# Performance work log

Hardware: AMD Instinct MI355X
Metric: run time of the kernel (lower is better)

The kernel has to match this reference:

```python
import jax, jax.numpy as jnp
import numpy as np

N_NODES = 65536
VOCAB = 1000
IN_DIM = 256
MEM_DIM = 256
HIDDEN = 256
NUM_CLASSES = 2


def _rand_parents(rng, n):
    # parent[i] < i for i >= 1 ; node 0 is the root (parent entry unused/masked)
    p = np.zeros(n, dtype=np.int64)
    p[1:] = rng.integers(0, np.arange(1, n))
    return jnp.asarray(p, dtype=jnp.int32)


def setup_inputs() -> dict:
    key = jax.random.key(0)
    ks = jax.random.split(key, 16)
    rng = np.random.default_rng(0)
    s = 0.05
    return {
        "l_tokens": jax.random.randint(ks[0], (N_NODES,), 0, VOCAB, dtype=jnp.int32),
        "l_parent": _rand_parents(rng, N_NODES),
        "r_tokens": jax.random.randint(ks[1], (N_NODES,), 0, VOCAB, dtype=jnp.int32),
        "r_parent": _rand_parents(rng, N_NODES),
        "emb_W": jax.random.normal(ks[2], (VOCAB, IN_DIM), jnp.float32) * s,
        "Wioux": jax.random.normal(ks[3], (IN_DIM, 3 * MEM_DIM), jnp.float32) * s,
        "bioux": jax.random.normal(ks[4], (3 * MEM_DIM,), jnp.float32) * s,
        "Wiouh": jax.random.normal(ks[5], (MEM_DIM, 3 * MEM_DIM), jnp.float32) * s,
        "biouh": jax.random.normal(ks[6], (3 * MEM_DIM,), jnp.float32) * s,
        "Wfx": jax.random.normal(ks[7], (IN_DIM, MEM_DIM), jnp.float32) * s,
        "bfx": jax.random.normal(ks[8], (MEM_DIM,), jnp.float32) * s,
        "Wfh": jax.random.normal(ks[9], (MEM_DIM, MEM_DIM), jnp.float32) * s,
        "bfh": jax.random.normal(ks[10], (MEM_DIM,), jnp.float32) * s,
        "Wh": jax.random.normal(ks[11], (2 * MEM_DIM, HIDDEN), jnp.float32) * s,
        "bh": jax.random.normal(ks[12], (HIDDEN,), jnp.float32) * s,
        "Wp": jax.random.normal(ks[13], (HIDDEN, NUM_CLASSES), jnp.float32) * s,
        "bp": jax.random.normal(ks[14], (NUM_CLASSES,), jnp.float32) * s,
    }


def _tree_lstm_root_c(tokens, parent, emb_W, Wioux, bioux, Wiouh, biouh,
                      Wfx, bfx, Wfh, bfh):
    # Batched x-dependent projections (faithful: ioux(emb), fx(emb))
    X = emb_W[tokens]                       # [N, in_dim]
    ioux_all = X @ Wioux + bioux            # [N, 3M]
    fx_all = X @ Wfx + bfx                  # [N, M]
    n = tokens.shape[0]
    m = Wfh.shape[0]

    def step(carry, i):
        h_sum, fc_sum, c_root = carry
        # ChildSumTreeLSTM.node_forward for node i
        iou = ioux_all[i] + h_sum[i] @ Wiouh + biouh
        ig, og, ug = jnp.split(iou, 3)
        c = jax.nn.sigmoid(ig) * jnp.tanh(ug) + fc_sum[i]   # leaf: fc_sum=0, h_sum=0
        h = jax.nn.sigmoid(og) * jnp.tanh(c)
        # forget-gate contribution of node i to its parent p:
        p = parent[i]
        f = jax.nn.sigmoid(h @ Wfh + bfh + fx_all[p])
        mask = (i != 0).astype(h.dtype)      # root has no parent
        h_sum = h_sum.at[p].add(h * mask)
        fc_sum = fc_sum.at[p].add(f * c * mask)
        c_root = jnp.where(i == 0, c, c_root)
        return (h_sum, fc_sum, c_root), None

    init = (jnp.zeros((n, m), X.dtype), jnp.zeros((n, m), X.dtype),
            jnp.zeros((m,), X.dtype))
    # children-before-parents order: descending index (parent[i] < i)
    (h_sum, fc_sum, c_root), _ = jax.lax.scan(step, init, jnp.arange(n - 1, -1, -1))
    return c_root                            # lstate == root cell state c


def reference(l_tokens, l_parent, r_tokens, r_parent, emb_W, Wioux, bioux,
              Wiouh, biouh, Wfx, bfx, Wfh, bfh, Wh, bh, Wp, bp):
    cl = _tree_lstm_root_c(l_tokens, l_parent, emb_W, Wioux, bioux, Wiouh,
                           biouh, Wfx, bfx, Wfh, bfh)
    cr = _tree_lstm_root_c(r_tokens, r_parent, emb_W, Wioux, bioux, Wiouh,
                           biouh, Wfx, bfx, Wfh, bfh)
    # Similarity head on root cell states
    vec = jnp.concatenate([cl * cr, jnp.abs(cl - cr)])[None, :]  # [1, 2M]
    hid = jax.nn.sigmoid(vec @ Wh + bh)
    return jax.nn.softmax(hid @ Wp + bp, axis=1)                 # [1, num_classes]
```

## Files before the change

### kernel.cpp

```cpp
#include <hip/hip_runtime.h>
#include <math.h>

#define NN 65536
#define TWO_N (2 * NN)
#define VOCAB 1000
#define MD 256
#define G3 768
#define DMAX 65536
#define HALF (DMAX / 2)
#define DCAP 128
#define NB 64
#define NT 256
#define NTS 1024
#define NSPAN 1024
#define SPAN 128
#define NTEAMS 64

typedef __attribute__((ext_vector_type(8))) short bf16x8;
typedef __attribute__((ext_vector_type(4))) float f32x4;

struct Params {
    const int* l_tokens; const int* l_parent;
    const int* r_tokens; const int* r_parent;
    const float* emb_W;
    const float* Wioux; const float* bioux;
    const float* Wiouh; const float* biouh;
    const float* Wfx;   const float* bfx;
    const float* Wfh;   const float* bfh;
    const float* Wh;    const float* bh;
    const float* Wp;    const float* bp;
    float* out;
    float* E_ioux;
    float* E_fx;
    float* C_leaf;
    float* H_leaf;
    float* FH_leaf;
    unsigned int* Wiouh_p;
    unsigned int* Wfh_p;
    float* h_sum;
    float* fc_sum;
    float* c_root;
    unsigned short* hstage;
    int* tarr;
    int* anc_a; int* anc_b; int* dep_a; int* dep_b;
    int* hc;
    int* pending;
    int* pend2;
    int* rank;
    int* blocksum;
    int* cnt; int* offs; int* cur;
    int* order;
    int* lorder;
    int* lstart;
    int* gtab;
    int* gdb;
    int* ecut;
    int* dbase;
    int* maxd;
    int cap_rows;
};

struct SWT {
    unsigned int wiou[12 * 2048];
    unsigned short hbufA[NB * MD];
    int nid[NB]; int row[NB]; int prow[NB]; int tok[NB]; int ptok[NB];
    int pgid[NB];
};

__device__ __forceinline__ float sigmoidf_(float x) {
    return 1.0f / (1.0f + __expf(-x));
}
__device__ __forceinline__ float tanhf_(float x) {
    float ex = __expf(2.0f * x);
    return 1.0f - 2.0f / (ex + 1.0f);
}
__device__ __forceinline__ unsigned int bf16rne_(float x) {
    unsigned int b = __float_as_uint(x);
    return (b + 0x7FFFu + ((b >> 16) & 1u)) >> 16;
}
__device__ __forceinline__ int aload_(int* p) {
    return __hip_atomic_load(p, __ATOMIC_RELAXED, __HIP_MEMORY_SCOPE_AGENT);
}
__device__ __forceinline__ float acohf_(const float* p) {
    return __hip_atomic_load((float*)p, __ATOMIC_RELAXED,
                             __HIP_MEMORY_SCOPE_AGENT);
}
__device__ __forceinline__ unsigned long long acohu64_(const void* p) {
    return __hip_atomic_load((unsigned long long*)p, __ATOMIC_RELAXED,
                             __HIP_MEMORY_SCOPE_AGENT);
}
__device__ __forceinline__ int rowr(const Params& P, int tree, int d, int lr) {
    int r = P.dbase[tree * HALF + d] + lr;
    if (r >= P.cap_rows) r -= P.cap_rows;
    return r;
}

__global__ __launch_bounds__(NT) void k_prep(Params P) {
    __shared__ float es[4][MD];
    const int t = threadIdx.x, bid = blockIdx.x, nblk = gridDim.x;
    const int gsize = nblk * NT, gtid = bid * NT + t;
    for (int u = gtid; u < 48 * 2048; u += gsize) {
        int tl = u >> 11, rem = u & 2047;
        int kb = rem >> 8, rem2 = rem & 255;
        int ln = rem2 >> 2, jj = (rem2 & 3) << 1;
        int k = kb * 32 + (ln >> 4) * 8 + jj;
        int n = tl * 16 + (ln & 15);
        float x0 = P.Wiouh[(size_t)k * G3 + n];
        float x1 = P.Wiouh[(size_t)(k + 1) * G3 + n];
        P.Wiouh_p[u] = bf16rne_(x0) | (bf16rne_(x1) << 16);
    }
    for (int u = gtid; u < 16 * 2048; u += gsize) {
        int tl = u >> 11, rem = u & 2047;
        int kb = rem >> 8, rem2 = rem & 255;
        int ln = rem2 >> 2, jj = (rem2 & 3) << 1;
        int k = kb * 32 + (ln >> 4) * 8 + jj;
        int n = tl * 16 + (ln & 15);
        float x0 = P.Wfh[(size_t)k * MD + n];
        float x1 = P.Wfh[(size_t)(k + 1) * MD + n];
        P.Wfh_p[u] = bf16rne_(x0) | (bf16rne_(x1) << 16);
    }
    for (int v0 = bid * 4; v0 < VOCAB; v0 += nblk * 4) {
        __syncthreads();
        #pragma unroll
        for (int r = 0; r < 4; ++r)
            es[r][t] = (v0 + r < VOCAB) ? P.emb_W[(size_t)(v0 + r) * MD + t] : 0.f;
        __syncthreads();
        float a0[4] = {0.f,0.f,0.f,0.f}, a1[4] = {0.f,0.f,0.f,0.f};
        float a2[4] = {0.f,0.f,0.f,0.f}, a3[4] = {0.f,0.f,0.f,0.f};
        for (int k = 0; k < MD; ++k) {
            float wi = P.Wioux[k * G3 + t];
            float wo = P.Wioux[k * G3 + 256 + t];
            float wu = P.Wioux[k * G3 + 512 + t];
            float wf = P.Wfx[k * MD + t];
            #pragma unroll
            for (int r = 0; r < 4; ++r) {
                float e = es[r][k];
                a0[r] += wi * e; a1[r] += wo * e; a2[r] += wu * e; a3[r] += wf * e;
            }
        }
        float bi = P.bioux[t], bo = P.bioux[256 + t], bu = P.bioux[512 + t], bf = P.bfx[t];
        float hb_i = P.biouh[t], hb_o = P.biouh[256 + t], hb_u = P.biouh[512 + t];
        __syncthreads();
        for (int r = 0; r < 4; ++r) {
            float hl = 0.f;
            if (v0 + r < VOCAB) {
                float ei = a0[r] + bi, eo = a1[r] + bo, eu = a2[r] + bu;
                P.E_ioux[(size_t)(v0 + r) * G3 + t]       = ei;
                P.E_ioux[(size_t)(v0 + r) * G3 + 256 + t] = eo;
                P.E_ioux[(size_t)(v0 + r) * G3 + 512 + t] = eu;
                P.E_fx[(size_t)(v0 + r) * MD + t]         = a3[r] + bf;
                float cl = sigmoidf_(ei + hb_i) * tanhf_(eu + hb_u);
                hl = sigmoidf_(eo + hb_o) * tanhf_(cl);
                P.C_leaf[(size_t)(v0 + r) * MD + t] = cl;
                P.H_leaf[(size_t)(v0 + r) * MD + t] = hl;
            }
            es[r][t] = hl;
        }
        __syncthreads();
        float af[4] = {0.f,0.f,0.f,0.f};
        for (int k = 0; k < MD; ++k) {
            float wf = P.Wfh[(size_t)k * MD + t];
            #pragma unroll
            for (int r = 0; r < 4; ++r) af[r] += wf * es[r][k];
        }
        for (int r = 0; r < 4; ++r)
            if (v0 + r < VOCAB) P.FH_leaf[(size_t)(v0 + r) * MD + t] = af[r];
        __syncthreads();
    }
    for (int g = gtid; g < TWO_N; g += gsize) {
        int tree = g >> 16, i = g & (NN - 1);
        if (i == 0) { P.anc_a[g] = g; P.dep_a[g] = 0; }
        else {
            const int* par = tree ? P.r_parent : P.l_parent;
            int pg = (tree << 16) | par[i];
            P.anc_a[g] = pg;
            P.dep_a[g] = 1;
            P.hc[pg] = 1;
        }
    }
}

__global__ __launch_bounds__(NT) void k_double(Params P, int it) {
    const int gtid = blockIdx.x * NT + threadIdx.x;
    const int gsize = gridDim.x * NT;
    if (it == 0) {
        for (int g = gtid; g < TWO_N; g += gsize) {
            int i = g & (NN - 1);
            if (i != 0 && !P.hc[g]) {
                int tree = g >> 16;
                const int* par = tree ? P.r_parent : P.l_parent;
                atomicAdd(&P.pending[(tree << 16) | par[i]], 1);
            }
        }
    }
    int* pa = (it & 1) ? P.anc_b : P.anc_a;
    int* pd = (it & 1) ? P.dep_b : P.dep_a;
    int* qa = (it & 1) ? P.anc_a : P.anc_b;
    int* qd = (it & 1) ? P.dep_a : P.dep_b;
    for (int g = gtid; g < TWO_N; g += gsize) {
        if (!P.hc[g]) continue;
        int a = pa[g];
        qd[g] = pd[g] + pd[a];
        qa[g] = pa[a];
    }
}

__global__ __launch_bounds__(NT) void k_s1(Params P) {
    __shared__ int hcnt[2 * DCAP];
    __shared__ int hmax2[2];
    const int t = threadIdx.x, bid = blockIdx.x, nblk = gridDim.x;
    const int gsize = nblk * NT, gtid = bid * NT + t;
    for (int i = t; i < 2 * DCAP; i += NT) hcnt[i] = 0;
    if (t < 2) hmax2[t] = 0;
    __syncthreads();
    for (int g = gtid; g < TWO_N; g += gsize) {
        if (!P.hc[g]) continue;
        int tree = g >> 16;
        int d = P.dep_a[g];
        if (d < DCAP) {
            atomicAdd(&hcnt[tree * DCAP + d], 1);
            atomicMax(&hmax2[tree], d);
        } else {
            atomicAdd(&P.cnt[tree * DMAX + d], 1);
            atomicMax(&P.maxd[tree], d);
        }
    }
    __syncthreads();
    for (int i = t; i < 2 * DCAP; i += NT) {
        int c = hcnt[i];
        if (c > 0) atomicAdd(&P.cnt[(i >= DCAP ? DMAX : 0) + (i & (DCAP - 1))], c);
    }
    if (t < 2) atomicMax(&P.maxd[t], hmax2[t]);
    for (int sp = bid; sp < NSPAN; sp += nblk) {
        __syncthreads();
        if (t < SPAN) hcnt[t] = P.pending[sp * SPAN + t];
        __syncthreads();
        for (int off = 1; off < SPAN; off <<= 1) {
            int a = (t >= off && t < SPAN) ? hcnt[t - off] : 0;
            __syncthreads();
            if (t < SPAN) hcnt[t] += a;
            __syncthreads();
        }
        if (t == SPAN - 1) P.blocksum[sp] = hcnt[t];
    }
}

__global__ __launch_bounds__(NT) void k_s2(Params P) {
    __shared__ int hcnt[NT];
    const int t = threadIdx.x;
    int4 v = ((const int4*)P.blocksum)[t];
    int s4 = v.x + v.y + v.z + v.w;
    hcnt[t] = s4;
    __syncthreads();
    for (int off = 1; off < NT; off <<= 1) {
        int a = (t >= off) ? hcnt[t - off] : 0;
        __syncthreads();
        hcnt[t] += a;
        __syncthreads();
    }
    int excl = t ? hcnt[t - 1] : 0;
    int4 r;
    r.x = excl; r.y = r.x + v.x; r.z = r.y + v.y; r.w = r.z + v.z;
    ((int4*)P.blocksum)[t] = r;
    if (t == NT - 1) P.maxd[23] = hcnt[NT - 1];
    __syncthreads();
    if (t < 2) {
        int tree = t;
        int run = tree * NN;
        int md = P.maxd[tree];
        for (int d = 0; d <= md; ++d) {
            P.offs[tree * DMAX + d] = run;
            run += P.cnt[tree * DMAX + d];
        }
    }
    __syncthreads();
    int md0 = P.maxd[0], md1 = P.maxd[1];
    int smax = md0 > md1 ? md0 : md1;
    if (t == 0) {
        long p = 0;
        for (int d = smax; d >= 0; --d) {
            P.dbase[d] = (int)(p % (long)P.cap_rows);
            p += P.cnt[d];
            P.dbase[HALF + d] = (int)(p % (long)P.cap_rows);
            p += P.cnt[DMAX + d];
        }
        int e = 0, hi = smax;
        while (hi >= 0) {
            long s = (long)(P.cnt[hi] + P.cnt[DMAX + hi]);
            if (hi > 0) s += P.cnt[hi - 1] + P.cnt[DMAX + hi - 1];
            int lo = hi;
            while (lo > 0) {
                long add = (lo - 1 > 0)
                    ? (P.cnt[lo - 2] + P.cnt[DMAX + lo - 2]) : 0;
                if (s + add > (long)P.cap_rows) break;
                s += add; --lo;
            }
            P.ecut[e++] = lo;
            hi = lo - 1;
        }
        P.maxd[24] = e;
        int j = 0;
        for (int d = smax; d >= 0; --d) {
            P.gdb[d] = j;
            j += (P.cnt[d] + NB - 1) / NB + (P.cnt[DMAX + d] + NB - 1) / NB;
        }
        P.maxd[22] = j;
    }
    __syncthreads();
    for (int d = t; d <= smax; d += NT) {
        int j = P.gdb[d];
        for (int tr = 0; tr < 2; ++tr) {
            int mdt = tr ? md1 : md0;
            int n = (d <= mdt) ? P.cnt[tr * DMAX + d] : 0;
            int st = P.offs[tr * DMAX + d];
            for (int b = 0; b < n; b += NB) {
                int cv = n - b; if (cv > NB) cv = NB;
                P.gtab[j++] = (st + b) | (cv << 20);
            }
        }
    }
}

__global__ __launch_bounds__(NT) void k_p2(Params P) {
    __shared__ int hcnt[NT];
    const int t = threadIdx.x, bid = blockIdx.x, nblk = gridDim.x;
    for (int sp = bid; sp < NSPAN; sp += nblk) {
        __syncthreads();
        if (t < SPAN) hcnt[t] = P.pending[sp * SPAN + t];
        __syncthreads();
        for (int off = 1; off < SPAN; off <<= 1) {
            int a = (t >= off && t < SPAN) ? hcnt[t - off] : 0;
            __syncthreads();
            if (t < SPAN) hcnt[t] += a;
            __syncthreads();
        }
        if (t < SPAN) {
            int excl = t ? hcnt[t - 1] : 0;
            P.lstart[sp * SPAN + t] = P.blocksum[sp] + excl;
        }
    }
}

__global__ __launch_bounds__(NT) void k_s3(Params P) {
    __shared__ int hcnt[2 * DCAP];
    __shared__ int hbase[2 * DCAP];
    const int t = threadIdx.x, bid = blockIdx.x, nblk = gridDim.x;
    const int gsize = nblk * NT, gtid = bid * NT + t;
    for (int i = t; i < 2 * DCAP; i += NT) hcnt[i] = 0;
    __syncthreads();
    for (int g = gtid; g < TWO_N; g += gsize) {
        if (!P.hc[g]) continue;
        int tree = g >> 16;
        int d = P.dep_a[g];
        if (d < DCAP) atomicAdd(&hcnt[tree * DCAP + d], 1);
    }
    __syncthreads();
    for (int i = t; i < 2 * DCAP; i += NT) {
        int c = hcnt[i];
        if (c > 0) {
            int idx = (i >= DCAP ? DMAX : 0) + (i & (DCAP - 1));
            hbase[i] = P.offs[idx] + atomicAdd(&P.cur[idx], c);
        }
        hcnt[i] = 0;
    }
    __syncthreads();
    for (int g = gtid; g < TWO_N; g += gsize) {
        int tree = g >> 16, i = g & (NN - 1);
        if (P.hc[g]) {
            int d = P.dep_a[g];
            if (d < DCAP) {
                int b = tree * DCAP + d;
                int pos = atomicAdd(&hcnt[b], 1);
                int gp = hbase[b] + pos;
                P.order[gp] = g;
                P.rank[g] = gp - P.offs[tree * DMAX + d];
            } else {
                int idx = tree * DMAX + d;
                int pos = atomicAdd(&P.cur[idx], 1);
                P.order[P.offs[idx] + pos] = g;
                P.rank[g] = pos;
            }
        } else if (i != 0) {
            const int* par = tree ? P.r_parent : P.l_parent;
            const int* toks = tree ? P.r_tokens : P.l_tokens;
            int pg = (tree << 16) | par[i];
            int pos = __hip_atomic_fetch_add(&P.pending[pg], -1,
                          __ATOMIC_RELAXED, __HIP_MEMORY_SCOPE_AGENT) - 1;
            P.lorder[P.lstart[pg] + pos] = toks[i];
        }
    }
}

__global__ __launch_bounds__(NT) void k_seed(Params P, int e) {
    const int t = threadIdx.x, bid = blockIdx.x, nblk = gridDim.x;
    int nep = P.maxd[24];
    if (e >= nep) return;
    int md0 = P.maxd[0], md1 = P.maxd[1];
    int smax = md0 > md1 ? md0 : md1;
    int hi = smax;
    for (int k = 0; k < e; ++k) hi = P.ecut[k] - 1;
    int lo = P.ecut[e];
    int sa = (lo > 0) ? lo - 1 : 0;
    int sb = (e == 0) ? hi : hi - 1;
    if (sa <= sb) {
        float b_f = P.bfh[t];
        for (int tree = 0; tree < 2; ++tree) {
            int mdt = tree ? md1 : md0;
            int bb = sb < mdt ? sb : mdt;
            if (sa > bb) continue;
            int st = P.offs[tree * DMAX + sa];
            int en = P.offs[tree * DMAX + bb] + P.cnt[tree * DMAX + bb];
            for (int idx = st + bid; idx < en; idx += nblk) {
                int g = P.order[idx];
                int i = g & (NN - 1);
                int tok = (tree ? P.r_tokens : P.l_tokens)[i];
                int d = P.dep_a[g];
                int row = rowr(P, tree, d, P.rank[g]);
                int ls = P.lstart[g];
                int le = (g + 1 < TWO_N) ? P.lstart[g + 1] : P.maxd[23];
                float efx = P.E_fx[(size_t)tok * MD + t] + b_f;
                float ha = 0.f, fa = 0.f;
                for (int k = ls; k < le; ++k) {
                    int lt = P.lorder[k];
                    ha += P.H_leaf[(size_t)lt * MD + t];
                    fa += sigmoidf_(P.FH_leaf[(size_t)lt * MD + t] + efx)
                          * P.C_leaf[(size_t)lt * MD + t];
                }
                P.h_sum[(size_t)row * MD + t] = ha;
                P.fc_sum[(size_t)row * MD + t] = fa;
            }
        }
    }
    if (e == 0) {
        const int gsize = nblk * NT, gtid = bid * NT + t;
        for (int g = gtid; g < TWO_N; g += gsize) {
            int i = g & (NN - 1);
            if (i != 0 && P.hc[g]) {
                int tree = g >> 16;
                const int* par = tree ? P.r_parent : P.l_parent;
                int pg = (tree << 16) | par[i];
                atomicAdd(&P.pending[pg], 4);
                atomicAdd(&P.pend2[pg], 4);
            }
        }
    }
}

__global__ __launch_bounds__(NTS, 1) void k_sweep(Params P, int e) {
    __shared__ SWT sm;
    int nep = P.maxd[24];
    if (e >= nep) return;
    const int t = threadIdx.x;
    const int b4 = blockIdx.x & 3;
    const int team = blockIdx.x >> 2;
    const int nteams = gridDim.x >> 2;
    const int wv = t >> 6;
    const int l = t & 63, lr = l >> 4, nloc = l & 15;

    for (int u = t; u < 12 * 2048; u += NTS) {
        int lt = u >> 11;
        int gate = lt >> 2, wq = lt & 3;
        sm.wiou[u] = P.Wiouh_p[(size_t)(gate * 16 + b4 * 4 + wq) * 2048 + (u & 2047)];
    }

    int md0 = P.maxd[0], md1 = P.maxd[1];
    int smax = md0 > md1 ? md0 : md1;
    int hi = smax;
    for (int k = 0; k < e; ++k) hi = P.ecut[k] - 1;
    int lo = P.ecut[e];
    int GT = P.maxd[22];
    int jend = (lo > 0) ? P.gdb[lo - 1] : GT;

    const unsigned short* Wl = (const unsigned short*)sm.wiou;
    const unsigned short* Wfg = (const unsigned short*)P.Wfh_p;
    int* tarr = P.tarr + e * NTEAMS + team;
    int kloc = 0;

    for (int j = P.gdb[hi] + team; j < jend; j += nteams, ++kloc) {
        int en = P.gtab[j];
        int base = en & 0xFFFFF, cntv = en >> 20;
        int nrb = (cntv + 15) >> 4;
        int ntask = nrb * 4;
        __syncthreads();
        if (t < NB) {
            int g = -1, row = 0, prow = 0, tok = 0, ptok = 0, pgid = 0;
            if (t < cntv) {
                g = P.order[base + t];
                int tree = g >> 16, i = g & (NN - 1);
                const int* toks = tree ? P.r_tokens : P.l_tokens;
                const int* pars = tree ? P.r_parent : P.l_parent;
                tok = toks[i];
                int d = P.dep_a[g];
                row = rowr(P, tree, d, P.rank[g]);
                if (i != 0) {
                    int pl = pars[i];
                    ptok = toks[pl];
                    pgid = (tree << 16) | pl;
                    prow = rowr(P, tree, d - 1, P.rank[pgid]);
                }
            }
            sm.nid[t] = g; sm.row[t] = row; sm.prow[t] = prow;
            sm.tok[t] = tok; sm.ptok[t] = ptok; sm.pgid[t] = pgid;
            if (g >= 0) {
                while (aload_(&P.pending[g]) != 0) __builtin_amdgcn_s_sleep(4);
            }
        }
        __syncthreads();

        const int mtot2 = (nrb << 4) * (MD / 2);
        for (int u = t; u < mtot2; u += NTS) {
            int m = u >> 7, c2 = (u & 127) << 1;
            unsigned int pk = 0;
            if (sm.nid[m] >= 0) {
                unsigned long long d2 =
                    acohu64_(&P.h_sum[(size_t)sm.row[m] * MD + c2]);
                float v0 = __uint_as_float((unsigned int)d2);
                float v1 = __uint_as_float((unsigned int)(d2 >> 32));
                pk = bf16rne_(v0) | (bf16rne_(v1) << 16);
            }
            *(unsigned int*)&sm.hbufA[m * MD + (c2 ^ ((m & 7) << 3))] = pk;
        }
        __syncthreads();

        f32x4 aiv, aov, auv;
        float crg[4];
        const int tt = wv;
        const int rb = tt >> 2, q = tt & 3;
        const int n = (b4 * 4 + q) * 16 + nloc;
        if (tt < ntask) {
            float b_i = P.biouh[n], b_o = P.biouh[256 + n], b_u = P.biouh[512 + n];
            #pragma unroll
            for (int r = 0; r < 4; ++r) {
                int m = rb * 16 + lr * 4 + r;
                float vi = 0.f, vo = 0.f, vu = 0.f;
                if (sm.nid[m] >= 0) {
                    const float* Ei = P.E_ioux + (size_t)sm.tok[m] * G3 + n;
                    vi = Ei[0] + b_i;
                    vo = Ei[256] + b_o;
                    vu = Ei[512] + b_u;
                }
                aiv[r] = vi; aov[r] = vo; auv[r] = vu;
            }
            #pragma unroll
            for (int kb = 0; kb < 8; ++kb) {
                int idx = (rb * 16 + nloc) * MD +
                          ((kb * 32 + lr * 8) ^ ((nloc & 7) << 3));
                bf16x8 afr = *(const bf16x8*)&sm.hbufA[idx];
                bf16x8 bi = *(const bf16x8*)&Wl[((q) * 8 + kb) * 512 + l * 8];
                bf16x8 bo = *(const bf16x8*)&Wl[((4 + q) * 8 + kb) * 512 + l * 8];
                bf16x8 bu = *(const bf16x8*)&Wl[((8 + q) * 8 + kb) * 512 + l * 8];
                aiv = __builtin_amdgcn_mfma_f32_16x16x32_bf16(afr, bi, aiv, 0, 0, 0);
                aov = __builtin_amdgcn_mfma_f32_16x16x32_bf16(afr, bo, aov, 0, 0, 0);
                auv = __builtin_amdgcn_mfma_f32_16x16x32_bf16(afr, bu, auv, 0, 0, 0);
            }
        }

        if (t < NB) {
            int g = sm.nid[t];
            if (g >= 0) {
                while (aload_(&P.pend2[g]) != 0) __builtin_amdgcn_s_sleep(4);
            }
        }
        __syncthreads();

        unsigned short* hs = P.hstage
            + ((size_t)(team * 2 + (kloc & 1))) * (NB * MD);
        if (tt < ntask) {
            #pragma unroll
            for (int r = 0; r < 4; ++r) {
                int m = rb * 16 + lr * 4 + r;
                int g = sm.nid[m];
                float c = 0.f, h = 0.f;
                if (g >= 0) {
                    float fcv = acohf_(&P.fc_sum[(size_t)sm.row[m] * MD + n]);
                    c = sigmoidf_(aiv[r]) * tanhf_(auv[r]) + fcv;
                    h = sigmoidf_(aov[r]) * tanhf_(c);
                    int i = g & (NN - 1);
                    if (i == 0) {
                        P.c_root[(g >> 16) * MD + n] = c;
                    } else {
                        atomicAdd(&P.h_sum[(size_t)sm.prow[m] * MD + n], h);
                    }
                }
                __hip_atomic_store(&hs[m * MD + n],
                                   (unsigned short)bf16rne_(h),
                                   __ATOMIC_RELAXED, __HIP_MEMORY_SCOPE_AGENT);
                crg[r] = c;
            }
        }

        __syncthreads();
        if (t < NB) {
            if (t == 0) {
                __hip_atomic_fetch_add(tarr, 1, __ATOMIC_RELAXED,
                                       __HIP_MEMORY_SCOPE_AGENT);
            }
            int g = sm.nid[t];
            if (g >= 0 && (g & (NN - 1)) != 0) {
                __hip_atomic_fetch_add(&P.pending[sm.pgid[t]], -1,
                                       __ATOMIC_RELAXED, __HIP_MEMORY_SCOPE_AGENT);
            }
        }
        if (t == 0) {
            while (aload_(tarr) < 4 * (kloc + 1)) __builtin_amdgcn_s_sleep(2);
        }
        __syncthreads();

        const unsigned long long* hs64 = (const unsigned long long*)hs;
        if (tt < ntask) {
            float b_f = P.bfh[n];
            f32x4 af;
            #pragma unroll
            for (int r = 0; r < 4; ++r) {
                int m = rb * 16 + lr * 4 + r;
                int g = sm.nid[m];
                float v = 0.f;
                if (g >= 0 && (g & (NN - 1)) != 0)
                    v = b_f + P.E_fx[(size_t)sm.ptok[m] * MD + n];
                af[r] = v;
            }
            #pragma unroll
            for (int kb = 0; kb < 8; ++kb) {
                union { unsigned long long u[2]; bf16x8 v; } hu;
                int u0 = ((rb * 16 + nloc) * 128 + (kb * 32 + lr * 8) / 2) >> 1;
                hu.u[0] = acohu64_(&hs64[u0]);
                hu.u[1] = acohu64_(&hs64[u0 + 1]);
                bf16x8 bf = *(const bf16x8*)&Wfg[(((b4 * 4 + q) * 8 + kb) * 64 + l) * 8];
                af = __builtin_amdgcn_mfma_f32_16x16x32_bf16(hu.v, bf, af, 0, 0, 0);
            }
            #pragma unroll
            for (int r = 0; r < 4; ++r) {
                int m = rb * 16 + lr * 4 + r;
                int g = sm.nid[m];
                if (g >= 0 && (g & (NN - 1)) != 0) {
                    atomicAdd(&P.fc_sum[(size_t)sm.prow[m] * MD + n],
                              sigmoidf_(af[r]) * crg[r]);
                }
            }
        }

        __syncthreads();
        if (t < NB) {
            int g = sm.nid[t];
            if (g >= 0 && (g & (NN - 1)) != 0) {
                __hip_atomic_fetch_add(&P.pend2[sm.pgid[t]], -1,
                                       __ATOMIC_RELAXED, __HIP_MEMORY_SCOPE_AGENT);
            }
        }
    }
}

__global__ __launch_bounds__(NT) void k_head(Params P) {
    __shared__ float vec[2 * MD];
    __shared__ float red[2][NT];
    const int t = threadIdx.x;
    float cl = P.c_root[t], cr = P.c_root[MD + t];
    vec[t] = cl * cr;
    vec[MD + t] = fabsf(cl - cr);
    __syncthreads();
    float acc = 0.f;
    for (int j = 0; j < 2 * MD; ++j) acc += vec[j] * P.Wh[(size_t)j * MD + t];
    float hid = sigmoidf_(acc + P.bh[t]);
    red[0][t] = hid * P.Wp[t * 2 + 0];
    red[1][t] = hid * P.Wp[t * 2 + 1];
    __syncthreads();
    for (int s = 128; s > 0; s >>= 1) {
        if (t < s) {
            red[0][t] += red[0][t + s];
            red[1][t] += red[1][t + s];
        }
        __syncthreads();
    }
    if (t == 0) {
        float l0 = red[0][0] + P.bp[0];
        float l1 = red[1][0] + P.bp[1];
        float mx = fmaxf(l0, l1);
        float e0 = __expf(l0 - mx), e1 = __expf(l1 - mx);
        float inv = 1.0f / (e0 + e1);
        P.out[0] = e0 * inv;
        P.out[1] = e1 * inv;
    }
}

extern "C" void kernel_launch(void* const* d_in, const int* in_sizes, int n_in,
                              void* d_out, int out_size, void* d_ws, size_t ws_size,
                              hipStream_t stream) {
    Params P;
    P.l_tokens = (const int*)d_in[0];
    P.l_parent = (const int*)d_in[1];
    P.r_tokens = (const int*)d_in[2];
    P.r_parent = (const int*)d_in[3];
    P.emb_W = (const float*)d_in[4];
    P.Wioux = (const float*)d_in[5];
    P.bioux = (const float*)d_in[6];
    P.Wiouh = (const float*)d_in[7];
    P.biouh = (const float*)d_in[8];
    P.Wfx   = (const float*)d_in[9];
    P.bfx   = (const float*)d_in[10];
    P.Wfh   = (const float*)d_in[11];
    P.bfh   = (const float*)d_in[12];
    P.Wh    = (const float*)d_in[13];
    P.bh    = (const float*)d_in[14];
    P.Wp    = (const float*)d_in[15];
    P.bp    = (const float*)d_in[16];
    P.out   = (float*)d_out;

    char* w = (char*)d_ws;
    auto alloc = [&](size_t bytes) {
        char* r = w;
        w += (bytes + 255) & ~(size_t)255;
        return r;
    };
    P.E_ioux   = (float*)alloc((size_t)VOCAB * G3 * 4);
    P.E_fx     = (float*)alloc((size_t)VOCAB * MD * 4);
    P.C_leaf   = (float*)alloc((size_t)VOCAB * MD * 4);
    P.H_leaf   = (float*)alloc((size_t)VOCAB * MD * 4);
    P.FH_leaf  = (float*)alloc((size_t)VOCAB * MD * 4);
    P.Wiouh_p  = (unsigned int*)alloc((size_t)48 * 2048 * 4);
    P.Wfh_p    = (unsigned int*)alloc((size_t)16 * 2048 * 4);
    P.c_root   = (float*)alloc(2 * MD * 4);
    P.hstage   = (unsigned short*)alloc((size_t)NTEAMS * 2 * NB * MD * 2);
    P.tarr     = (int*)alloc((size_t)8 * NTEAMS * 4);
    P.anc_a    = (int*)alloc((size_t)TWO_N * 4);
    P.dep_a    = (int*)alloc((size_t)TWO_N * 4);
    P.hc       = (int*)alloc((size_t)TWO_N * 4);
    P.pending  = (int*)alloc((size_t)TWO_N * 4);
    P.pend2    = (int*)alloc((size_t)TWO_N * 4);
    P.cnt      = (int*)alloc((size_t)2 * DMAX * 4);
    P.offs     = (int*)alloc((size_t)2 * DMAX * 4);
    P.cur      = (int*)alloc((size_t)2 * DMAX * 4);
    P.order    = (int*)alloc((size_t)TWO_N * 4);
    P.rank     = (int*)alloc((size_t)TWO_N * 4);
    P.lorder   = (int*)alloc((size_t)TWO_N * 4);
    P.blocksum = (int*)alloc((size_t)NSPAN * 4);
    P.gtab     = (int*)alloc((size_t)(TWO_N / 16 + 2 * DMAX + 256) * 4);
    P.gdb      = (int*)alloc((size_t)DMAX * 4);
    P.ecut     = (int*)alloc((size_t)DMAX * 4);
    P.dbase    = (int*)alloc((size_t)DMAX * 4);
    P.maxd     = (int*)alloc(256);
    P.anc_b = P.order;
    P.dep_b = P.rank;
    P.lstart = P.anc_a;

    size_t used = (size_t)(w - (char*)d_ws);
    size_t remain = (ws_size > used) ? (ws_size - used) : 0;
    size_t cap = remain / ((size_t)2 * MD * 4);
    if (cap > (size_t)TWO_N) cap = TWO_N;
    P.cap_rows = (int)cap;
    P.h_sum  = (float*)w;
    P.fc_sum = P.h_sum + cap * MD;

    hipMemsetAsync(P.hc, 0, (size_t)3 * TWO_N * 4, stream);
    hipMemsetAsync(P.cnt, 0, (size_t)3 * 2 * DMAX * 4, stream);
    hipMemsetAsync(P.maxd, 0, 256, stream);
    hipMemsetAsync(P.tarr, 0, (size_t)8 * NTEAMS * 4, stream);

    k_prep<<<dim3(512), dim3(NT), 0, stream>>>(P);
    for (int it = 0; it < 8; ++it)
        k_double<<<dim3(512), dim3(NT), 0, stream>>>(P, it);
    k_s1<<<dim3(NSPAN), dim3(NT), 0, stream>>>(P);
    k_s2<<<dim3(1), dim3(NT), 0, stream>>>(P);
    k_p2<<<dim3(NSPAN), dim3(NT), 0, stream>>>(P);
    k_s3<<<dim3(NSPAN), dim3(NT), 0, stream>>>(P);

    for (int e = 0; e < 6; ++e) {
        k_seed<<<dim3(1024), dim3(NT), 0, stream>>>(P, e);
        k_sweep<<<dim3(4 * NTEAMS), dim3(NTS), 0, stream>>>(P, e);
    }
    k_head<<<dim3(1), dim3(NT), 0, stream>>>(P);
}
```

Baseline: 957.8 us.

## Pack ancestor/depth into 64-bit words and prefetch sweep metadata double-buffered

Pointer-jumping now stores ancestor and depth together in one 64-bit word, so each doubling step needs two 8-byte loads and one store instead of four separate int loads and two stores. The sweep kernel double-buffers per-group node metadata in shared memory and loads the next group's metadata before waiting on the team barrier, which takes those dependent global loads off the critical path. This adds workspace for separate ad_a/ad_b and lstart buffers, which used to alias other arrays, and slightly more shared memory. A leading __syncthreads was also removed, so the buffer handoff relies on the existing barriers.

```diff
diff --git a/kernel.cpp b/kernel.cpp
--- a/kernel.cpp
+++ b/kernel.cpp
@@ -42,16 +42,17 @@
     float* c_root;
     unsigned short* hstage;
     int* tarr;
-    int* anc_a; int* anc_b; int* dep_a; int* dep_b;
+    unsigned long long* ad_a;
+    unsigned long long* ad_b;
     int* hc;
     int* pending;
     int* pend2;
     int* rank;
+    int* lstart;
     int* blocksum;
     int* cnt; int* offs; int* cur;
     int* order;
     int* lorder;
-    int* lstart;
     int* gtab;
     int* gdb;
     int* ecut;
@@ -63,8 +64,8 @@
 struct SWT {
     unsigned int wiou[12 * 2048];
     unsigned short hbufA[NB * MD];
-    int nid[NB]; int row[NB]; int prow[NB]; int tok[NB]; int ptok[NB];
-    int pgid[NB];
+    int nid[2][NB]; int row[2][NB]; int prow[2][NB];
+    int tok[2][NB]; int ptok[2][NB]; int pgid[2][NB];
 };
 
 __device__ __forceinline__ float sigmoidf_(float x) {
@@ -88,6 +89,9 @@
 __device__ __forceinline__ unsigned long long acohu64_(const void* p) {
     return __hip_atomic_load((unsigned long long*)p, __ATOMIC_RELAXED,
                              __HIP_MEMORY_SCOPE_AGENT);
+}
+__device__ __forceinline__ int dep_(const Params& P, int g) {
+    return ((const int*)P.ad_a)[2 * g];
 }
 __device__ __forceinline__ int rowr(const Params& P, int tree, int d, int lr) {
     int r = P.dbase[tree * HALF + d] + lr;
@@ -169,12 +173,12 @@
     }
     for (int g = gtid; g < TWO_N; g += gsize) {
         int tree = g >> 16, i = g & (NN - 1);
-        if (i == 0) { P.anc_a[g] = g; P.dep_a[g] = 0; }
-        else {
+        if (i == 0) {
+            P.ad_a[g] = ((unsigned long long)g << 32);
+        } else {
             const int* par = tree ? P.r_parent : P.l_parent;
             int pg = (tree << 16) | par[i];
-            P.anc_a[g] = pg;
-            P.dep_a[g] = 1;
+            P.ad_a[g] = ((unsigned long long)pg << 32) | 1ull;
             P.hc[pg] = 1;
         }
     }
@@ -193,15 +197,14 @@
             }
         }
     }
-    int* pa = (it & 1) ? P.anc_b : P.anc_a;
-    int* pd = (it & 1) ? P.dep_b : P.dep_a;
-    int* qa = (it & 1) ? P.anc_a : P.anc_b;
-    int* qd = (it & 1) ? P.dep_a : P.dep_b;
+    unsigned long long* pa = (it & 1) ? P.ad_b : P.ad_a;
+    unsigned long long* q  = (it & 1) ? P.ad_a : P.ad_b;
     for (int g = gtid; g < TWO_N; g += gsize) {
         if (!P.hc[g]) continue;
-        int a = pa[g];
-        qd[g] = pd[g] + pd[a];
-        qa[g] = pa[a];
+        unsigned long long v = pa[g];
+        unsigned long long va = pa[v >> 32];
+        q[g] = (va & 0xFFFFFFFF00000000ull)
+             | (unsigned long long)((unsigned int)v + (unsigned int)va);
     }
 }
 
@@ -216,7 +219,7 @@
     for (int g = gtid; g < TWO_N; g += gsize) {
         if (!P.hc[g]) continue;
         int tree = g >> 16;
-        int d = P.dep_a[g];
+        int d = dep_(P, g);
         if (d < DCAP) {
             atomicAdd(&hcnt[tree * DCAP + d], 1);
             atomicMax(&hmax2[tree], d);
@@ -351,7 +354,7 @@
     for (int g = gtid; g < TWO_N; g += gsize) {
         if (!P.hc[g]) continue;
         int tree = g >> 16;
-        int d = P.dep_a[g];
+        int d = dep_(P, g);
         if (d < DCAP) atomicAdd(&hcnt[tree * DCAP + d], 1);
     }
     __syncthreads();
@@ -367,7 +370,7 @@
     for (int g = gtid; g < TWO_N; g += gsize) {
         int tree = g >> 16, i = g & (NN - 1);
         if (P.hc[g]) {
-            int d = P.dep_a[g];
+            int d = dep_(P, g);
             if (d < DCAP) {
                 int b = tree * DCAP + d;
                 int pos = atomicAdd(&hcnt[b], 1);
@@ -414,7 +417,7 @@
                 int g = P.order[idx];
                 int i = g & (NN - 1);
                 int tok = (tree ? P.r_tokens : P.l_tokens)[i];
-                int d = P.dep_a[g];
+                int d = dep_(P, g);
                 int row = rowr(P, tree, d, P.rank[g]);
                 int ls = P.lstart[g];
                 int le = (g + 1 < TWO_N) ? P.lstart[g + 1] : P.maxd[23];
@@ -446,6 +449,32 @@
     }
 }
 
+__device__ __forceinline__ void load_meta(const Params& P, SWT& sm, int jj,
+                                          int buf, int t) {
+    if (t < NB) {
+        int g = -1, row = 0, prow = 0, tok = 0, ptok = 0, pgid = 0;
+        int en = P.gtab[jj];
+        int base = en & 0xFFFFF, cntv = en >> 20;
+        if (t < cntv) {
+            g = P.order[base + t];
+            int tree = g >> 16, i = g & (NN - 1);
+            const int* toks = tree ? P.r_tokens : P.l_tokens;
+            const int* pars = tree ? P.r_parent : P.l_parent;
+            tok = toks[i];
+            int d = dep_(P, g);
+            row = rowr(P, tree, d, P.rank[g]);
+            if (i != 0) {
+                int pl = pars[i];
+                ptok = toks[pl];
+                pgid = (tree << 16) | pl;
+                prow = rowr(P, tree, d - 1, P.rank[pgid]);
+            }
+        }
+        sm.nid[buf][t] = g; sm.row[buf][t] = row; sm.prow[buf][t] = prow;
+        sm.tok[buf][t] = tok; sm.ptok[buf][t] = ptok; sm.pgid[buf][t] = pgid;
+    }
+}
+
 __global__ __launch_bounds__(NTS, 1) void k_sweep(Params P, int e) {
     __shared__ SWT sm;
     int nep = P.maxd[24];
@@ -475,32 +504,18 @@
     const unsigned short* Wfg = (const unsigned short*)P.Wfh_p;
     int* tarr = P.tarr + e * NTEAMS + team;
     int kloc = 0;
-
-    for (int j = P.gdb[hi] + team; j < jend; j += nteams, ++kloc) {
+    int cur = 0;
+
+    const int j0 = P.gdb[hi] + team;
+    if (j0 < jend) load_meta(P, sm, j0, 0, t);
+
+    for (int j = j0; j < jend; j += nteams, ++kloc) {
         int en = P.gtab[j];
-        int base = en & 0xFFFFF, cntv = en >> 20;
+        int cntv = en >> 20;
         int nrb = (cntv + 15) >> 4;
         int ntask = nrb * 4;
-        __syncthreads();
         if (t < NB) {
-            int g = -1, row = 0, prow = 0, tok = 0, ptok = 0, pgid = 0;
-            if (t < cntv) {
-                g = P.order[base + t];
-                int tree = g >> 16, i = g & (NN - 1);
-                const int* toks = tree ? P.r_tokens : P.l_tokens;
-                const int* pars = tree ? P.r_parent : P.l_parent;
-                tok = toks[i];
-                int d = P.dep_a[g];
-                row = rowr(P, tree, d, P.rank[g]);
-                if (i != 0) {
-                    int pl = pars[i];
-                    ptok = toks[pl];
-                    pgid = (tree << 16) | pl;
-                    prow = rowr(P, tree, d - 1, P.rank[pgid]);
-                }
-            }
-            sm.nid[t] = g; sm.row[t] = row; sm.prow[t] = prow;
-            sm.tok[t] = tok; sm.ptok[t] = ptok; sm.pgid[t] = pgid;
+            int g = sm.nid[cur][t];
             if (g >= 0) {
                 while (aload_(&P.pending[g]) != 0) __builtin_amdgcn_s_sleep(4);
             }
@@ -511,9 +526,9 @@
         for (int u = t; u < mtot2; u += NTS) {
             int m = u >> 7, c2 = (u & 127) << 1;
             unsigned int pk = 0;
-            if (sm.nid[m] >= 0) {
+            if (sm.nid[cur][m] >= 0) {
                 unsigned long long d2 =
-                    acohu64_(&P.h_sum[(size_t)sm.row[m] * MD + c2]);
+                    acohu64_(&P.h_sum[(size_t)sm.row[cur][m] * MD + c2]);
                 float v0 = __uint_as_float((unsigned int)d2);
                 float v1 = __uint_as_float((unsigned int)(d2 >> 32));
                 pk = bf16rne_(v0) | (bf16rne_(v1) << 16);
@@ -533,8 +548,8 @@
             for (int r = 0; r < 4; ++r) {
                 int m = rb * 16 + lr * 4 + r;
                 float vi = 0.f, vo = 0.f, vu = 0.f;
-                if (sm.nid[m] >= 0) {
-                    const float* Ei = P.E_ioux + (size_t)sm.tok[m] * G3 + n;
+                if (sm.nid[cur][m] >= 0) {
+                    const float* Ei = P.E_ioux + (size_t)sm.tok[cur][m] * G3 + n;
                     vi = Ei[0] + b_i;
                     vo = Ei[256] + b_o;
                     vu = Ei[512] + b_u;
@@ -556,7 +571,7 @@
         }
 
         if (t < NB) {
-            int g = sm.nid[t];
+            int g = sm.nid[cur][t];
             if (g >= 0) {
                 while (aload_(&P.pend2[g]) != 0) __builtin_amdgcn_s_sleep(4);
             }
@@ -569,17 +584,17 @@
             #pragma unroll
             for (int r = 0; r < 4; ++r) {
                 int m = rb * 16 + lr * 4 + r;
-                int g = sm.nid[m];
+                int g = sm.nid[cur][m];
                 float c = 0.f, h = 0.f;
                 if (g >= 0) {
-                    float fcv = acohf_(&P.fc_sum[(size_t)sm.row[m] * MD + n]);
+                    float fcv = acohf_(&P.fc_sum[(size_t)sm.row[cur][m] * MD + n]);
                     c = sigmoidf_(aiv[r]) * tanhf_(auv[r]) + fcv;
                     h = sigmoidf_(aov[r]) * tanhf_(c);
                     int i = g & (NN - 1);
                     if (i == 0) {
                         P.c_root[(g >> 16) * MD + n] = c;
                     } else {
-                        atomicAdd(&P.h_sum[(size_t)sm.prow[m] * MD + n], h);
+                        atomicAdd(&P.h_sum[(size_t)sm.prow[cur][m] * MD + n], h);
                     }
                 }
                 __hip_atomic_store(&hs[m * MD + n],
@@ -595,12 +610,13 @@
                 __hip_atomic_fetch_add(tarr, 1, __ATOMIC_RELAXED,
                                        __HIP_MEMORY_SCOPE_AGENT);
             }
-            int g = sm.nid[t];
+            int g = sm.nid[cur][t];
             if (g >= 0 && (g & (NN - 1)) != 0) {
-                __hip_atomic_fetch_add(&P.pending[sm.pgid[t]], -1,
+                __hip_atomic_fetch_add(&P.pending[sm.pgid[cur][t]], -1,
                                        __ATOMIC_RELAXED, __HIP_MEMORY_SCOPE_AGENT);
             }
         }
+        if (j + nteams < jend) load_meta(P, sm, j + nteams, cur ^ 1, t);
         if (t == 0) {
             while (aload_(tarr) < 4 * (kloc + 1)) __builtin_amdgcn_s_sleep(2);
         }
@@ -613,10 +629,10 @@
             #pragma unroll
             for (int r = 0; r < 4; ++r) {
                 int m = rb * 16 + lr * 4 + r;
-                int g = sm.nid[m];
+                int g = sm.nid[cur][m];
                 float v = 0.f;
                 if (g >= 0 && (g & (NN - 1)) != 0)
-                    v = b_f + P.E_fx[(size_t)sm.ptok[m] * MD + n];
+                    v = b_f + P.E_fx[(size_t)sm.ptok[cur][m] * MD + n];
                 af[r] = v;
             }
             #pragma unroll
@@ -631,9 +647,9 @@
             #pragma unroll
             for (int r = 0; r < 4; ++r) {
                 int m = rb * 16 + lr * 4 + r;
-                int g = sm.nid[m];
+                int g = sm.nid[cur][m];
                 if (g >= 0 && (g & (NN - 1)) != 0) {
-                    atomicAdd(&P.fc_sum[(size_t)sm.prow[m] * MD + n],
+                    atomicAdd(&P.fc_sum[(size_t)sm.prow[cur][m] * MD + n],
                               sigmoidf_(af[r]) * crg[r]);
                 }
             }
@@ -641,12 +657,13 @@
 
         __syncthreads();
         if (t < NB) {
-            int g = sm.nid[t];
+            int g = sm.nid[cur][t];
             if (g >= 0 && (g & (NN - 1)) != 0) {
-                __hip_atomic_fetch_add(&P.pend2[sm.pgid[t]], -1,
+                __hip_atomic_fetch_add(&P.pend2[sm.pgid[cur][t]], -1,
                                        __ATOMIC_RELAXED, __HIP_MEMORY_SCOPE_AGENT);
             }
         }
+        cur ^= 1;
     }
 }
 
@@ -721,8 +738,8 @@
     P.c_root   = (float*)alloc(2 * MD * 4);
     P.hstage   = (unsigned short*)alloc((size_t)NTEAMS * 2 * NB * MD * 2);
     P.tarr     = (int*)alloc((size_t)8 * NTEAMS * 4);
-    P.anc_a    = (int*)alloc((size_t)TWO_N * 4);
-    P.dep_a    = (int*)alloc((size_t)TWO_N * 4);
+    P.ad_a     = (unsigned long long*)alloc((size_t)TWO_N * 8);
+    P.ad_b     = (unsigned long long*)alloc((size_t)TWO_N * 8);
     P.hc       = (int*)alloc((size_t)TWO_N * 4);
     P.pending  = (int*)alloc((size_t)TWO_N * 4);
     P.pend2    = (int*)alloc((size_t)TWO_N * 4);
@@ -731,6 +748,7 @@
     P.cur      = (int*)alloc((size_t)2 * DMAX * 4);
     P.order    = (int*)alloc((size_t)TWO_N * 4);
     P.rank     = (int*)alloc((size_t)TWO_N * 4);
+    P.lstart   = (int*)alloc((size_t)TWO_N * 4);
     P.lorder   = (int*)alloc((size_t)TWO_N * 4);
     P.blocksum = (int*)alloc((size_t)NSPAN * 4);
     P.gtab     = (int*)alloc((size_t)(TWO_N / 16 + 2 * DMAX + 256) * 4);
@@ -738,9 +756,6 @@
     P.ecut     = (int*)alloc((size_t)DMAX * 4);
     P.dbase    = (int*)alloc((size_t)DMAX * 4);
     P.maxd     = (int*)alloc(256);
-    P.anc_b = P.order;
-    P.dep_b = P.rank;
-    P.lstart = P.anc_a;
 
     size_t used = (size_t)(w - (char*)d_ws);
     size_t remain = (ws_size > used) ? (ws_size - used) : 0;
```

Measured after the change: 912.3 us. 1.05x faster.
